# Performance work log

Measured on AMD Instinct MI355X. Metric: run time of the kernel, lower is better.

## Reference

```python
import jax, jax.numpy as jnp
import numpy as np

NUM_HEADS = 32
NUM_KV_HEADS = 8
HEAD_DIM = 128
SEQ = 2048
MAX_SLOTS = 4096
SCALE = float(1.0 / np.sqrt(HEAD_DIM))  # attn_scale
G = NUM_HEADS // NUM_KV_HEADS  # num_queries_per_kv


def setup_inputs() -> dict:
    key = jax.random.key(0)
    k1, k2, k3 = jax.random.split(key, 3)
    q = jax.random.normal(k1, (SEQ, NUM_HEADS, HEAD_DIM), dtype=jnp.float32)
    k = jax.random.normal(k2, (SEQ, NUM_KV_HEADS, HEAD_DIM), dtype=jnp.float32)
    v = jax.random.normal(k3, (SEQ, NUM_KV_HEADS, HEAD_DIM), dtype=jnp.float32)
    k_cache = jnp.zeros((MAX_SLOTS, NUM_KV_HEADS, HEAD_DIM), dtype=jnp.float32)
    v_cache = jnp.zeros((MAX_SLOTS, NUM_KV_HEADS, HEAD_DIM), dtype=jnp.float32)
    slot_mapping = jnp.arange(SEQ, dtype=jnp.int64)  # contiguous block_table slots
    return {"q": q, "k": k, "v": v, "k_cache": k_cache, "v_cache": v_cache,
            "slot_mapping": slot_mapping}


def reference(q, k, v, k_cache, v_cache, slot_mapping):
    # prefill: scatter-write new K/V into the paged cache (self.k_cache[slot_mapping] = k)
    kc = k_cache.at[slot_mapping].set(k)
    vc = v_cache.at[slot_mapping].set(v)
    # gather K/V back from the cache via slot mapping (paged gather pattern)
    k_attn = kc[slot_mapping]  # (S, Hkv, D) == k since slots are unique
    v_attn = vc[slot_mapping]
    # GQA: repeat_interleave kv heads to match query heads
    kr = jnp.repeat(k_attn, G, axis=1)  # (S, H, D)
    vr = jnp.repeat(v_attn, G, axis=1)
    # scores: (H, Sq, Sk), naive full materialization as in the original
    scores = jnp.einsum('qhd,khd->hqk', q, kr) * SCALE
    sq, sk = q.shape[0], k_attn.shape[0]
    mask = jnp.tril(jnp.ones((sq, sk), dtype=bool))  # causal (num_query_tokens > 1)
    scores = jnp.where(mask[None, :, :], scores, -jnp.inf)
    weights = jax.nn.softmax(scores, axis=-1)
    out = jnp.einsum('hqk,khd->qhd', weights, vr)  # (S, H, D)
    return out
```

## Files before the change

kernel.cpp:

```cpp
#include <hip/hip_runtime.h>
#include <hip/hip_bf16.h>

#define SEQ 2048
#define QSTR 4096
#define CSCALE 0.1275174364688796f

typedef __attribute__((ext_vector_type(8)))  short short8;
typedef __attribute__((ext_vector_type(4)))  float f32x4;
typedef __attribute__((ext_vector_type(16))) float f32x16;

union PF8 { unsigned u[4]; short8 s; };

__device__ __forceinline__ unsigned short f2bf(float f) {
    union { __hip_bfloat16 b; unsigned short u; } cv;
    cv.b = __float2bfloat16(f);
    return cv.u;
}
__device__ __forceinline__ float bf2f(unsigned short u) {
    unsigned v = ((unsigned)u) << 16;
    return __builtin_bit_cast(float, v);
}

__device__ __forceinline__ void gload16(const unsigned short* g, unsigned short* l) {
    __builtin_amdgcn_global_load_lds(
        (const __attribute__((address_space(1))) void*)g,
        (__attribute__((address_space(3))) void*)l, 16, 0, 0);
}

__global__ void prep_k(const float* __restrict__ Kg, unsigned short* __restrict__ Kb) {
    int gi = blockIdx.x * 256 + threadIdx.x;
    int kv = gi >> 8;
    int rem = gi & 255;
    int hk = rem >> 5;
    int d4 = rem & 31;
    f32x4 k4 = *(const f32x4*)(Kg + ((size_t)kv * 8 + hk) * 128 + 4 * d4);
    ushort4 u = make_ushort4(f2bf(k4[0]), f2bf(k4[1]), f2bf(k4[2]), f2bf(k4[3]));
    *(ushort4*)(Kb + ((size_t)hk * SEQ + kv) * 128 + 4 * d4) = u;
}

__global__ void prep_v(const float* __restrict__ Vg, unsigned short* __restrict__ Vtb) {
    const int hk  = blockIdx.x >> 5;
    const int kvb = blockIdx.x & 31;
    __shared__ unsigned short T[128][72];
    const int t = threadIdx.x;
    #pragma unroll
    for (int i = 0; i < 8; ++i) {
        int idx = t + 256 * i;
        int r = idx >> 5, d4 = idx & 31;
        f32x4 v = *(const f32x4*)(Vg + ((size_t)(kvb * 64 + r) * 8 + hk) * 128 + 4 * d4);
        T[4 * d4 + 0][r] = f2bf(v[0]);
        T[4 * d4 + 1][r] = f2bf(v[1]);
        T[4 * d4 + 2][r] = f2bf(v[2]);
        T[4 * d4 + 3][r] = f2bf(v[3]);
    }
    __syncthreads();
    #pragma unroll
    for (int i = 0; i < 8; ++i) {
        int idx = t + 256 * i;
        int d = idx >> 4, c4 = idx & 15;
        ushort4 u = *(ushort4*)&T[d][4 * c4];
        *(ushort4*)(Vtb + ((size_t)hk * 128 + d) * SEQ + kvb * 64 + 4 * c4) = u;
    }
}

__launch_bounds__(256, 2)
__global__ void attn_fwd(const float* __restrict__ Qg,
                         const unsigned short* __restrict__ Kb,
                         const unsigned short* __restrict__ Vtb,
                         float* __restrict__ Og) {
    const int bid = blockIdx.x;
    const int p   = bid >> 5;
    const int h   = bid & 31;
    const int hk  = h >> 2;
    const int qbB = 31 - p;
    const int qbA = p;
    const int nsB = 32 - p;

    const int tid  = threadIdx.x;
    const int w    = tid >> 6;
    const int b    = w & 1;
    const int hf   = w >> 1;
    const int lane = tid & 63;
    const int q5   = lane & 31;
    const int t5   = lane >> 5;

    __shared__ unsigned short Ks[2][64][128];
    __shared__ unsigned short Vp[2][64][128];
    __shared__ float mstat[2][4][32];
    __shared__ unsigned short Otb[32][136];

    short8 qf[8];
    auto LOADQ = [&](int qb) __attribute__((always_inline)) {
        const float* qp = Qg + (size_t)(qb * 64 + 32 * b + q5) * QSTR + h * 128 + 8 * t5;
        #pragma unroll
        for (int st = 0; st < 8; ++st) {
            f32x4 a = *(const f32x4*)(qp + 16 * st);
            f32x4 c = *(const f32x4*)(qp + 16 * st + 4);
            short8 f;
            f[0] = (short)f2bf(a[0] * CSCALE); f[1] = (short)f2bf(a[1] * CSCALE);
            f[2] = (short)f2bf(a[2] * CSCALE); f[3] = (short)f2bf(a[3] * CSCALE);
            f[4] = (short)f2bf(c[0] * CSCALE); f[5] = (short)f2bf(c[1] * CSCALE);
            f[6] = (short)f2bf(c[2] * CSCALE); f[7] = (short)f2bf(c[3] * CSCALE);
            qf[st] = f;
        }
    };

    auto ISSUE = [&](int kv0, int bb) __attribute__((always_inline)) {
        #pragma unroll
        for (int p4 = 0; p4 < 4; ++p4) {
            int row = 16 * w + 4 * p4 + (lane >> 4);
            const unsigned short* g = Kb +
                ((size_t)hk * SEQ + kv0 + row) * 128 + 8 * ((lane & 15) ^ (row & 15));
            gload16(g, &Ks[bb][16 * w + 4 * p4][0]);
        }
        #pragma unroll
        for (int p4 = 0; p4 < 4; ++p4) {
            int r  = 16 * w + 4 * p4 + (lane >> 4);
            int gg = lane & 15;
            int d  = 2 * r + (gg >> 3);
            int c  = (gg & 7) ^ (r & 7);
            const unsigned short* g = Vtb +
                ((size_t)hk * 128 + d) * SEQ + kv0 + 8 * c;
            gload16(g, &Vp[bb][16 * w + 4 * p4][0]);
        }
    };

    f32x16 oacc[4];
    float m, l;
    auto RESET = [&]() __attribute__((always_inline)) {
        #pragma unroll
        for (int dt = 0; dt < 4; ++dt)
            #pragma unroll
            for (int r = 0; r < 16; ++r) oacc[dt][r] = 0.f;
        m = -1e30f; l = 0.f;
    };

    auto EPI = [&](int qb) __attribute__((always_inline)) {
        if (t5 == 0) mstat[0][w][q5] = m;
        asm volatile("s_waitcnt lgkmcnt(0)" ::: "memory");
        __builtin_amdgcn_sched_barrier(0);
        __builtin_amdgcn_s_barrier();
        const float mo = mstat[0][w ^ 2][q5];
        const float M  = fmaxf(m, mo);
        const float sc = exp2f(m - M);
        #pragma unroll
        for (int dt = 0; dt < 4; ++dt)
            #pragma unroll
            for (int r = 0; r < 16; ++r) oacc[dt][r] *= sc;
        const float lp = l * sc;
        if (t5 == 0) mstat[1][w][q5] = lp;
        asm volatile("s_waitcnt lgkmcnt(0)" ::: "memory");
        __builtin_amdgcn_sched_barrier(0);
        __builtin_amdgcn_s_barrier();
        const float rl = 1.0f / (lp + mstat[1][w ^ 2][q5]);

        #pragma unroll 1
        for (int bb = 0; bb < 2; ++bb) {
            if (w == 2 + bb) {
                #pragma unroll
                for (int dt = 0; dt < 4; ++dt)
                    #pragma unroll
                    for (int ii = 0; ii < 4; ++ii) {
                        ushort4 u = make_ushort4(
                            f2bf(oacc[dt][4 * ii + 0]), f2bf(oacc[dt][4 * ii + 1]),
                            f2bf(oacc[dt][4 * ii + 2]), f2bf(oacc[dt][4 * ii + 3]));
                        *(ushort4*)&Otb[q5][32 * dt + 8 * ii + 4 * t5] = u;
                    }
            }
            asm volatile("s_waitcnt lgkmcnt(0)" ::: "memory");
            __builtin_amdgcn_sched_barrier(0);
            __builtin_amdgcn_s_barrier();
            if (w == bb) {
                #pragma unroll
                for (int dt = 0; dt < 4; ++dt)
                    #pragma unroll
                    for (int ii = 0; ii < 4; ++ii) {
                        ushort4 o1 = *(ushort4*)&Otb[q5][32 * dt + 8 * ii + 4 * t5];
                        ushort4 u = make_ushort4(
                            f2bf((oacc[dt][4 * ii + 0] + bf2f(o1.x)) * rl),
                            f2bf((oacc[dt][4 * ii + 1] + bf2f(o1.y)) * rl),
                            f2bf((oacc[dt][4 * ii + 2] + bf2f(o1.z)) * rl),
                            f2bf((oacc[dt][4 * ii + 3] + bf2f(o1.w)) * rl));
                        *(ushort4*)&Otb[q5][32 * dt + 8 * ii + 4 * t5] = u;
                    }
            }
            asm volatile("s_waitcnt lgkmcnt(0)" ::: "memory");
            __builtin_amdgcn_sched_barrier(0);
            __builtin_amdgcn_s_barrier();
            {
                const int r  = tid >> 3;
                const int c0 = 16 * (tid & 7);
                float* og = Og + (size_t)(qb * 64 + 32 * bb + r) * QSTR + h * 128 + c0;
                #pragma unroll
                for (int j = 0; j < 4; ++j) {
                    ushort4 u = *(ushort4*)&Otb[r][c0 + 4 * j];
                    f32x4 v;
                    v[0] = bf2f(u.x); v[1] = bf2f(u.y);
                    v[2] = bf2f(u.z); v[3] = bf2f(u.w);
                    *(f32x4*)(og + 4 * j) = v;
                }
            }
            asm volatile("s_waitcnt lgkmcnt(0)" ::: "memory");
            __builtin_amdgcn_sched_barrier(0);
            __builtin_amdgcn_s_barrier();
        }
    };

    LOADQ(qbB);
    #pragma unroll
    for (int st = 0; st < 8; ++st) asm volatile("" :: "v"(qf[st]));
    asm volatile("s_waitcnt vmcnt(0)" ::: "memory");
    RESET();

    ISSUE(0, 0);
    ISSUE(64, 1);

    for (int s = 0; s < 33; ++s) {
        if (s == nsB) {
            LOADQ(qbA);
            EPI(qbB);
            RESET();
        }
        const bool isB = (s < nsB);
        const int kv0  = isB ? 64 * s : 64 * (s - nsB);
        const int qb   = isB ? qbB : qbA;
        const int q0w  = qb * 64 + 32 * b;
        const int buf  = s & 1;

        if (s + 1 < 33) asm volatile("s_waitcnt vmcnt(8)" ::: "memory");
        else            asm volatile("s_waitcnt vmcnt(0)" ::: "memory");
        __builtin_amdgcn_s_barrier();

        const int kvh = kv0 + 32 * hf;
        if (kvh <= q0w + 31) {
            f32x16 sac;
            #pragma unroll
            for (int r = 0; r < 16; ++r) sac[r] = 0.f;
            __builtin_amdgcn_s_setprio(1);
            #pragma unroll
            for (int st = 0; st < 8; ++st) {
                short8 kf = *(const short8*)
                    &Ks[buf][32 * hf + q5][8 * ((2 * st + t5) ^ (q5 & 15))];
                sac = __builtin_amdgcn_mfma_f32_32x32x16_bf16(kf, qf[st], sac, 0, 0, 0);
            }
            __builtin_amdgcn_s_setprio(0);

            if (kvh + 31 > q0w) {
                const int qrow = q0w + q5;
                #pragma unroll
                for (int r = 0; r < 16; ++r) {
                    int kv = kvh + (r & 3) + 8 * (r >> 2) + 4 * t5;
                    if (kv > qrow) sac[r] = -1e30f;
                }
            }

            float m8[8], m4[4], m2[2];
            #pragma unroll
            for (int i = 0; i < 8; ++i) m8[i] = fmaxf(sac[i], sac[i + 8]);
            #pragma unroll
            for (int i = 0; i < 4; ++i) m4[i] = fmaxf(m8[i], m8[i + 4]);
            m2[0] = fmaxf(m4[0], m4[2]); m2[1] = fmaxf(m4[1], m4[3]);
            float mx = fmaxf(m2[0], m2[1]);
            mx = fmaxf(mx, __shfl_xor(mx, 32));

            const bool skip = __all(mx <= m + 11.0f);
            float fac = 1.0f;
            if (!skip) {
                float mn = fmaxf(m, mx);
                fac = exp2f(m - mn);
                m = mn;
            }

            #pragma unroll
            for (int r = 0; r < 16; ++r) sac[r] = exp2f(sac[r] - m);
            float s8[8], s4[4], s2[2];
            #pragma unroll
            for (int i = 0; i < 8; ++i) s8[i] = sac[i] + sac[i + 8];
            #pragma unroll
            for (int i = 0; i < 4; ++i) s4[i] = s8[i] + s8[i + 4];
            s2[0] = s4[0] + s4[2]; s2[1] = s4[1] + s4[3];
            float ps = s2[0] + s2[1];
            ps += __shfl_xor(ps, 32);
            if (!skip) {
                l = l * fac + ps;
                #pragma unroll
                for (int dt = 0; dt < 4; ++dt)
                    #pragma unroll
                    for (int r = 0; r < 16; ++r) oacc[dt][r] *= fac;
            } else {
                l += ps;
            }

            unsigned pkw[8];
            #pragma unroll
            for (int rp = 0; rp < 8; ++rp)
                pkw[rp] = (unsigned)f2bf(sac[2 * rp]) |
                          ((unsigned)f2bf(sac[2 * rp + 1]) << 16);

            unsigned xp[8];
            #pragma unroll
            for (int i = 0; i < 8; ++i)
                xp[i] = (unsigned)__shfl_xor((int)pkw[i], 32);

            PF8 pf[2];
            #pragma unroll
            for (int ks = 0; ks < 2; ++ks) {
                #pragma unroll
                for (int j = 0; j < 4; ++j) {
                    const int ib = (j & 1) + 4 * ks;
                    const unsigned own_lo = pkw[ib];
                    const unsigned own_hi = pkw[ib + 2];
                    const unsigned par_lo = xp[ib];
                    const unsigned par_hi = xp[ib + 2];
                    pf[ks].u[j] = (j < 2) ? (t5 ? par_hi : own_lo)
                                          : (t5 ? own_hi : par_lo);
                }
            }

            __builtin_amdgcn_s_setprio(1);
            #pragma unroll
            for (int dt = 0; dt < 4; ++dt) {
                #pragma unroll
                for (int ks = 0; ks < 2; ++ks) {
                    const int gg = 8 * (q5 & 1) +
                        ((4 * hf + 2 * ks + t5) ^ ((q5 >> 1) & 7));
                    short8 vf = *(const short8*)
                        &Vp[buf][16 * dt + (q5 >> 1)][8 * gg];
                    oacc[dt] = __builtin_amdgcn_mfma_f32_32x32x16_bf16(vf, pf[ks].s, oacc[dt], 0, 0, 0);
                }
            }
            __builtin_amdgcn_s_setprio(0);
        }

        asm volatile("" ::: "memory");
        __builtin_amdgcn_s_barrier();
        if (s + 2 < 33) {
            const int s2 = s + 2;
            ISSUE((s2 < nsB) ? 64 * s2 : 64 * (s2 - nsB), s & 1);
        }
    }

    EPI(qbA);
}

extern "C" void kernel_launch(void* const* d_in, const int* in_sizes, int n_in,
                              void* d_out, int out_size, void* d_ws, size_t ws_size,
                              hipStream_t stream) {
    const float* q = (const float*)d_in[0];
    const float* k = (const float*)d_in[1];
    const float* v = (const float*)d_in[2];
    float* out = (float*)d_out;
    unsigned short* Kb  = (unsigned short*)d_ws;
    unsigned short* Vtb = Kb + (size_t)8 * SEQ * 128;
    prep_k<<<dim3(2048), 256, 0, stream>>>(k, Kb);
    prep_v<<<dim3(256), 256, 0, stream>>>(v, Vtb);
    attn_fwd<<<dim3(512), 256, 0, stream>>>(q, Kb, Vtb, out);
}
```

Baseline: 90.90 us.

## Switch attention MFMAs from 32x32x16 to 16x16x32 tiles with reworked fragment layouts

Replaces the 32x32x16 bf16 MFMA tiling for both QK^T and PV with 16x16x32 MFMAs, splitting each wave's 32 query rows into two 16-row halves that keep separate max and sum statistics. The Q, K and V fragment loads, the causal mask indexing, the softmax reductions (now two-level shuffles) and the P repacking via cross-lane shuffles are all rewritten for the new layout, and K fragments are loaded into registers ahead of the MFMAs. The aim is a cheaper instruction mix or better MFMA issue and latency behaviour. In exchange it adds more shuffles and register pressure, and a risk of layout mismatches.

```diff
diff --git a/kernel.cpp b/kernel.cpp
--- a/kernel.cpp
+++ b/kernel.cpp
@@ -7,7 +7,6 @@
 
 typedef __attribute__((ext_vector_type(8)))  short short8;
 typedef __attribute__((ext_vector_type(4)))  float f32x4;
-typedef __attribute__((ext_vector_type(16))) float f32x16;
 
 union PF8 { unsigned u[4]; short8 s; };
 
@@ -81,27 +80,31 @@
     const int b    = w & 1;
     const int hf   = w >> 1;
     const int lane = tid & 63;
-    const int q5   = lane & 31;
-    const int t5   = lane >> 5;
+    const int c16  = lane & 15;
+    const int g    = lane >> 4;
 
     __shared__ unsigned short Ks[2][64][128];
     __shared__ unsigned short Vp[2][64][128];
     __shared__ float mstat[2][4][32];
     __shared__ unsigned short Otb[32][136];
 
-    short8 qf[8];
+    short8 qf[2][4];
     auto LOADQ = [&](int qb) __attribute__((always_inline)) {
-        const float* qp = Qg + (size_t)(qb * 64 + 32 * b + q5) * QSTR + h * 128 + 8 * t5;
-        #pragma unroll
-        for (int st = 0; st < 8; ++st) {
-            f32x4 a = *(const f32x4*)(qp + 16 * st);
-            f32x4 c = *(const f32x4*)(qp + 16 * st + 4);
-            short8 f;
-            f[0] = (short)f2bf(a[0] * CSCALE); f[1] = (short)f2bf(a[1] * CSCALE);
-            f[2] = (short)f2bf(a[2] * CSCALE); f[3] = (short)f2bf(a[3] * CSCALE);
-            f[4] = (short)f2bf(c[0] * CSCALE); f[5] = (short)f2bf(c[1] * CSCALE);
-            f[6] = (short)f2bf(c[2] * CSCALE); f[7] = (short)f2bf(c[3] * CSCALE);
-            qf[st] = f;
+        #pragma unroll
+        for (int hf2 = 0; hf2 < 2; ++hf2) {
+            const float* qp = Qg + (size_t)(qb * 64 + 32 * b + 16 * hf2 + c16) * QSTR
+                              + h * 128 + 8 * g;
+            #pragma unroll
+            for (int kt = 0; kt < 4; ++kt) {
+                f32x4 a = *(const f32x4*)(qp + 32 * kt);
+                f32x4 c = *(const f32x4*)(qp + 32 * kt + 4);
+                short8 f;
+                f[0] = (short)f2bf(a[0] * CSCALE); f[1] = (short)f2bf(a[1] * CSCALE);
+                f[2] = (short)f2bf(a[2] * CSCALE); f[3] = (short)f2bf(a[3] * CSCALE);
+                f[4] = (short)f2bf(c[0] * CSCALE); f[5] = (short)f2bf(c[1] * CSCALE);
+                f[6] = (short)f2bf(c[2] * CSCALE); f[7] = (short)f2bf(c[3] * CSCALE);
+                qf[hf2][kt] = f;
+            }
         }
     };
 
@@ -109,9 +112,9 @@
         #pragma unroll
         for (int p4 = 0; p4 < 4; ++p4) {
             int row = 16 * w + 4 * p4 + (lane >> 4);
-            const unsigned short* g = Kb +
+            const unsigned short* gp = Kb +
                 ((size_t)hk * SEQ + kv0 + row) * 128 + 8 * ((lane & 15) ^ (row & 15));
-            gload16(g, &Ks[bb][16 * w + 4 * p4][0]);
+            gload16(gp, &Ks[bb][16 * w + 4 * p4][0]);
         }
         #pragma unroll
         for (int p4 = 0; p4 < 4; ++p4) {
@@ -119,52 +122,59 @@
             int gg = lane & 15;
             int d  = 2 * r + (gg >> 3);
             int c  = (gg & 7) ^ (r & 7);
-            const unsigned short* g = Vtb +
+            const unsigned short* gp = Vtb +
                 ((size_t)hk * 128 + d) * SEQ + kv0 + 8 * c;
-            gload16(g, &Vp[bb][16 * w + 4 * p4][0]);
+            gload16(gp, &Vp[bb][16 * w + 4 * p4][0]);
         }
     };
 
-    f32x16 oacc[4];
-    float m, l;
+    f32x4 o4[2][8];
+    float m[2], l[2];
     auto RESET = [&]() __attribute__((always_inline)) {
         #pragma unroll
-        for (int dt = 0; dt < 4; ++dt)
-            #pragma unroll
-            for (int r = 0; r < 16; ++r) oacc[dt][r] = 0.f;
-        m = -1e30f; l = 0.f;
+        for (int hf2 = 0; hf2 < 2; ++hf2)
+            #pragma unroll
+            for (int dt = 0; dt < 8; ++dt)
+                o4[hf2][dt] = (f32x4){0.f, 0.f, 0.f, 0.f};
+        m[0] = m[1] = -1e30f; l[0] = l[1] = 0.f;
     };
 
     auto EPI = [&](int qb) __attribute__((always_inline)) {
-        if (t5 == 0) mstat[0][w][q5] = m;
+        if (g == 0) { mstat[0][w][c16] = m[0]; mstat[0][w][16 + c16] = m[1]; }
         asm volatile("s_waitcnt lgkmcnt(0)" ::: "memory");
         __builtin_amdgcn_sched_barrier(0);
         __builtin_amdgcn_s_barrier();
-        const float mo = mstat[0][w ^ 2][q5];
-        const float M  = fmaxf(m, mo);
-        const float sc = exp2f(m - M);
-        #pragma unroll
-        for (int dt = 0; dt < 4; ++dt)
-            #pragma unroll
-            for (int r = 0; r < 16; ++r) oacc[dt][r] *= sc;
-        const float lp = l * sc;
-        if (t5 == 0) mstat[1][w][q5] = lp;
+        float lp[2], rl[2];
+        #pragma unroll
+        for (int hf2 = 0; hf2 < 2; ++hf2) {
+            const float mo = mstat[0][w ^ 2][16 * hf2 + c16];
+            const float M  = fmaxf(m[hf2], mo);
+            const float sc = exp2f(m[hf2] - M);
+            #pragma unroll
+            for (int dt = 0; dt < 8; ++dt)
+                #pragma unroll
+                for (int r = 0; r < 4; ++r) o4[hf2][dt][r] *= sc;
+            lp[hf2] = l[hf2] * sc;
+        }
+        if (g == 0) { mstat[1][w][c16] = lp[0]; mstat[1][w][16 + c16] = lp[1]; }
         asm volatile("s_waitcnt lgkmcnt(0)" ::: "memory");
         __builtin_amdgcn_sched_barrier(0);
         __builtin_amdgcn_s_barrier();
-        const float rl = 1.0f / (lp + mstat[1][w ^ 2][q5]);
+        #pragma unroll
+        for (int hf2 = 0; hf2 < 2; ++hf2)
+            rl[hf2] = 1.0f / (lp[hf2] + mstat[1][w ^ 2][16 * hf2 + c16]);
 
         #pragma unroll 1
         for (int bb = 0; bb < 2; ++bb) {
             if (w == 2 + bb) {
                 #pragma unroll
-                for (int dt = 0; dt < 4; ++dt)
-                    #pragma unroll
-                    for (int ii = 0; ii < 4; ++ii) {
+                for (int hf2 = 0; hf2 < 2; ++hf2)
+                    #pragma unroll
+                    for (int dt = 0; dt < 8; ++dt) {
                         ushort4 u = make_ushort4(
-                            f2bf(oacc[dt][4 * ii + 0]), f2bf(oacc[dt][4 * ii + 1]),
-                            f2bf(oacc[dt][4 * ii + 2]), f2bf(oacc[dt][4 * ii + 3]));
-                        *(ushort4*)&Otb[q5][32 * dt + 8 * ii + 4 * t5] = u;
+                            f2bf(o4[hf2][dt][0]), f2bf(o4[hf2][dt][1]),
+                            f2bf(o4[hf2][dt][2]), f2bf(o4[hf2][dt][3]));
+                        *(ushort4*)&Otb[16 * hf2 + c16][16 * dt + 4 * g] = u;
                     }
             }
             asm volatile("s_waitcnt lgkmcnt(0)" ::: "memory");
@@ -172,16 +182,16 @@
             __builtin_amdgcn_s_barrier();
             if (w == bb) {
                 #pragma unroll
-                for (int dt = 0; dt < 4; ++dt)
-                    #pragma unroll
-                    for (int ii = 0; ii < 4; ++ii) {
-                        ushort4 o1 = *(ushort4*)&Otb[q5][32 * dt + 8 * ii + 4 * t5];
+                for (int hf2 = 0; hf2 < 2; ++hf2)
+                    #pragma unroll
+                    for (int dt = 0; dt < 8; ++dt) {
+                        ushort4 o1 = *(ushort4*)&Otb[16 * hf2 + c16][16 * dt + 4 * g];
                         ushort4 u = make_ushort4(
-                            f2bf((oacc[dt][4 * ii + 0] + bf2f(o1.x)) * rl),
-                            f2bf((oacc[dt][4 * ii + 1] + bf2f(o1.y)) * rl),
-                            f2bf((oacc[dt][4 * ii + 2] + bf2f(o1.z)) * rl),
-                            f2bf((oacc[dt][4 * ii + 3] + bf2f(o1.w)) * rl));
-                        *(ushort4*)&Otb[q5][32 * dt + 8 * ii + 4 * t5] = u;
+                            f2bf((o4[hf2][dt][0] + bf2f(o1.x)) * rl[hf2]),
+                            f2bf((o4[hf2][dt][1] + bf2f(o1.y)) * rl[hf2]),
+                            f2bf((o4[hf2][dt][2] + bf2f(o1.z)) * rl[hf2]),
+                            f2bf((o4[hf2][dt][3] + bf2f(o1.w)) * rl[hf2]));
+                        *(ushort4*)&Otb[16 * hf2 + c16][16 * dt + 4 * g] = u;
                     }
             }
             asm volatile("s_waitcnt lgkmcnt(0)" ::: "memory");
@@ -208,7 +218,9 @@
 
     LOADQ(qbB);
     #pragma unroll
-    for (int st = 0; st < 8; ++st) asm volatile("" :: "v"(qf[st]));
+    for (int hf2 = 0; hf2 < 2; ++hf2)
+        #pragma unroll
+        for (int kt = 0; kt < 4; ++kt) asm volatile("" :: "v"(qf[hf2][kt]));
     asm volatile("s_waitcnt vmcnt(0)" ::: "memory");
     RESET();
 
@@ -233,101 +245,120 @@
 
         const int kvh = kv0 + 32 * hf;
         if (kvh <= q0w + 31) {
-            f32x16 sac;
-            #pragma unroll
-            for (int r = 0; r < 16; ++r) sac[r] = 0.f;
+            short8 kf[8];
+            #pragma unroll
+            for (int ct = 0; ct < 2; ++ct)
+                #pragma unroll
+                for (int kt = 0; kt < 4; ++kt)
+                    kf[4 * ct + kt] = *(const short8*)
+                        &Ks[buf][32 * hf + 16 * ct + c16][8 * ((4 * kt + g) ^ c16)];
+
+            f32x4 sac[2][2];
+            #pragma unroll
+            for (int hf2 = 0; hf2 < 2; ++hf2)
+                #pragma unroll
+                for (int ct = 0; ct < 2; ++ct)
+                    sac[hf2][ct] = (f32x4){0.f, 0.f, 0.f, 0.f};
             __builtin_amdgcn_s_setprio(1);
             #pragma unroll
-            for (int st = 0; st < 8; ++st) {
-                short8 kf = *(const short8*)
-                    &Ks[buf][32 * hf + q5][8 * ((2 * st + t5) ^ (q5 & 15))];
-                sac = __builtin_amdgcn_mfma_f32_32x32x16_bf16(kf, qf[st], sac, 0, 0, 0);
+            for (int kt = 0; kt < 4; ++kt) {
+                sac[0][0] = __builtin_amdgcn_mfma_f32_16x16x32_bf16(kf[kt],     qf[0][kt], sac[0][0], 0, 0, 0);
+                sac[1][0] = __builtin_amdgcn_mfma_f32_16x16x32_bf16(kf[kt],     qf[1][kt], sac[1][0], 0, 0, 0);
+                sac[0][1] = __builtin_amdgcn_mfma_f32_16x16x32_bf16(kf[4 + kt], qf[0][kt], sac[0][1], 0, 0, 0);
+                sac[1][1] = __builtin_amdgcn_mfma_f32_16x16x32_bf16(kf[4 + kt], qf[1][kt], sac[1][1], 0, 0, 0);
             }
             __builtin_amdgcn_s_setprio(0);
 
             if (kvh + 31 > q0w) {
-                const int qrow = q0w + q5;
-                #pragma unroll
-                for (int r = 0; r < 16; ++r) {
-                    int kv = kvh + (r & 3) + 8 * (r >> 2) + 4 * t5;
-                    if (kv > qrow) sac[r] = -1e30f;
+                #pragma unroll
+                for (int hf2 = 0; hf2 < 2; ++hf2) {
+                    const int qrow = q0w + 16 * hf2 + c16;
+                    #pragma unroll
+                    for (int ct = 0; ct < 2; ++ct)
+                        #pragma unroll
+                        for (int r = 0; r < 4; ++r) {
+                            int kv = kvh + 16 * ct + 4 * g + r;
+                            if (kv > qrow) sac[hf2][ct][r] = -1e30f;
+                        }
                 }
             }
 
-            float m8[8], m4[4], m2[2];
-            #pragma unroll
-            for (int i = 0; i < 8; ++i) m8[i] = fmaxf(sac[i], sac[i + 8]);
-            #pragma unroll
-            for (int i = 0; i < 4; ++i) m4[i] = fmaxf(m8[i], m8[i + 4]);
-            m2[0] = fmaxf(m4[0], m4[2]); m2[1] = fmaxf(m4[1], m4[3]);
-            float mx = fmaxf(m2[0], m2[1]);
-            mx = fmaxf(mx, __shfl_xor(mx, 32));
-
-            const bool skip = __all(mx <= m + 11.0f);
-            float fac = 1.0f;
+            float mx[2];
+            #pragma unroll
+            for (int hf2 = 0; hf2 < 2; ++hf2) {
+                float t4a = fmaxf(sac[hf2][0][0], sac[hf2][1][0]);
+                float t4b = fmaxf(sac[hf2][0][1], sac[hf2][1][1]);
+                float t4c = fmaxf(sac[hf2][0][2], sac[hf2][1][2]);
+                float t4d = fmaxf(sac[hf2][0][3], sac[hf2][1][3]);
+                float t2a = fmaxf(t4a, t4b), t2b = fmaxf(t4c, t4d);
+                float mm = fmaxf(t2a, t2b);
+                mm = fmaxf(mm, __shfl_xor(mm, 16));
+                mm = fmaxf(mm, __shfl_xor(mm, 32));
+                mx[hf2] = mm;
+            }
+
+            const bool skip = __all(fmaxf(mx[0] - m[0], mx[1] - m[1]) <= 11.0f);
             if (!skip) {
-                float mn = fmaxf(m, mx);
-                fac = exp2f(m - mn);
-                m = mn;
-            }
-
-            #pragma unroll
-            for (int r = 0; r < 16; ++r) sac[r] = exp2f(sac[r] - m);
-            float s8[8], s4[4], s2[2];
-            #pragma unroll
-            for (int i = 0; i < 8; ++i) s8[i] = sac[i] + sac[i + 8];
-            #pragma unroll
-            for (int i = 0; i < 4; ++i) s4[i] = s8[i] + s8[i + 4];
-            s2[0] = s4[0] + s4[2]; s2[1] = s4[1] + s4[3];
-            float ps = s2[0] + s2[1];
-            ps += __shfl_xor(ps, 32);
-            if (!skip) {
-                l = l * fac + ps;
-                #pragma unroll
-                for (int dt = 0; dt < 4; ++dt)
-                    #pragma unroll
-                    for (int r = 0; r < 16; ++r) oacc[dt][r] *= fac;
-            } else {
-                l += ps;
-            }
-
-            unsigned pkw[8];
-            #pragma unroll
-            for (int rp = 0; rp < 8; ++rp)
-                pkw[rp] = (unsigned)f2bf(sac[2 * rp]) |
-                          ((unsigned)f2bf(sac[2 * rp + 1]) << 16);
-
-            unsigned xp[8];
-            #pragma unroll
-            for (int i = 0; i < 8; ++i)
-                xp[i] = (unsigned)__shfl_xor((int)pkw[i], 32);
-
-            PF8 pf[2];
-            #pragma unroll
-            for (int ks = 0; ks < 2; ++ks) {
-                #pragma unroll
-                for (int j = 0; j < 4; ++j) {
-                    const int ib = (j & 1) + 4 * ks;
-                    const unsigned own_lo = pkw[ib];
-                    const unsigned own_hi = pkw[ib + 2];
-                    const unsigned par_lo = xp[ib];
-                    const unsigned par_hi = xp[ib + 2];
-                    pf[ks].u[j] = (j < 2) ? (t5 ? par_hi : own_lo)
-                                          : (t5 ? own_hi : par_lo);
+                #pragma unroll
+                for (int hf2 = 0; hf2 < 2; ++hf2) {
+                    float mn  = fmaxf(m[hf2], mx[hf2]);
+                    float fac = exp2f(m[hf2] - mn);
+                    m[hf2] = mn;
+                    l[hf2] *= fac;
+                    #pragma unroll
+                    for (int dt = 0; dt < 8; ++dt)
+                        #pragma unroll
+                        for (int r = 0; r < 4; ++r) o4[hf2][dt][r] *= fac;
                 }
             }
 
+            unsigned pk[2][4];
+            #pragma unroll
+            for (int hf2 = 0; hf2 < 2; ++hf2) {
+                #pragma unroll
+                for (int ct = 0; ct < 2; ++ct)
+                    #pragma unroll
+                    for (int r = 0; r < 4; ++r)
+                        sac[hf2][ct][r] = exp2f(sac[hf2][ct][r] - m[hf2]);
+                float s4a = sac[hf2][0][0] + sac[hf2][1][0];
+                float s4b = sac[hf2][0][1] + sac[hf2][1][1];
+                float s4c = sac[hf2][0][2] + sac[hf2][1][2];
+                float s4d = sac[hf2][0][3] + sac[hf2][1][3];
+                float ps = (s4a + s4b) + (s4c + s4d);
+                ps += __shfl_xor(ps, 16);
+                ps += __shfl_xor(ps, 32);
+                l[hf2] += ps;
+                #pragma unroll
+                for (int ct = 0; ct < 2; ++ct)
+                    #pragma unroll
+                    for (int pp = 0; pp < 2; ++pp)
+                        pk[hf2][2 * ct + pp] =
+                            (unsigned)f2bf(sac[hf2][ct][2 * pp]) |
+                            ((unsigned)f2bf(sac[hf2][ct][2 * pp + 1]) << 16);
+            }
+
+            PF8 pf0, pf1;
+            {
+                const int sel = g >> 1;
+                #pragma unroll
+                for (int w4 = 0; w4 < 4; ++w4) {
+                    const int src = 16 * (2 * (g & 1) + (w4 >> 1)) + c16;
+                    unsigned lo0 = (unsigned)__shfl((int)pk[0][w4 & 1], src);
+                    unsigned hi0 = (unsigned)__shfl((int)pk[0][2 + (w4 & 1)], src);
+                    unsigned lo1 = (unsigned)__shfl((int)pk[1][w4 & 1], src);
+                    unsigned hi1 = (unsigned)__shfl((int)pk[1][2 + (w4 & 1)], src);
+                    pf0.u[w4] = sel ? hi0 : lo0;
+                    pf1.u[w4] = sel ? hi1 : lo1;
+                }
+            }
+
             __builtin_amdgcn_s_setprio(1);
             #pragma unroll
-            for (int dt = 0; dt < 4; ++dt) {
-                #pragma unroll
-                for (int ks = 0; ks < 2; ++ks) {
-                    const int gg = 8 * (q5 & 1) +
-                        ((4 * hf + 2 * ks + t5) ^ ((q5 >> 1) & 7));
-                    short8 vf = *(const short8*)
-                        &Vp[buf][16 * dt + (q5 >> 1)][8 * gg];
-                    oacc[dt] = __builtin_amdgcn_mfma_f32_32x32x16_bf16(vf, pf[ks].s, oacc[dt], 0, 0, 0);
-                }
+            for (int dt = 0; dt < 8; ++dt) {
+                const int gg = 8 * (c16 & 1) + ((4 * hf + g) ^ (c16 >> 1));
+                short8 vf = *(const short8*)&Vp[buf][8 * dt + (c16 >> 1)][8 * gg];
+                o4[0][dt] = __builtin_amdgcn_mfma_f32_16x16x32_bf16(vf, pf0.s, o4[0][dt], 0, 0, 0);
+                o4[1][dt] = __builtin_amdgcn_mfma_f32_16x16x32_bf16(vf, pf1.s, o4[1][dt], 0, 0, 0);
             }
             __builtin_amdgcn_s_setprio(0);
         }
```

Result: slower. 99.90 us (+9.9%).

## Drop double-buffered K/V prefetch for single buffer to raise occupancy to three blocks

Applied to the files above, without the earlier changes.

Replaces the two-stage asynchronous K/V prefetch ring with a single LDS buffer that is loaded synchronously at the start of each iteration. LDS use per block drops, so the launch bound can request three blocks per CU instead of two. It also halves the cross-half-wave shuffles by sending only the half of each packed probability word the partner lane needs. In exchange, global load latency is no longer hidden inside a block and must be covered by the extra resident blocks.

```diff
diff --git a/kernel.cpp b/kernel.cpp
--- a/kernel.cpp
+++ b/kernel.cpp
@@ -63,7 +63,7 @@
     }
 }
 
-__launch_bounds__(256, 2)
+__launch_bounds__(256, 3)
 __global__ void attn_fwd(const float* __restrict__ Qg,
                          const unsigned short* __restrict__ Kb,
                          const unsigned short* __restrict__ Vtb,
@@ -84,8 +84,8 @@
     const int q5   = lane & 31;
     const int t5   = lane >> 5;
 
-    __shared__ unsigned short Ks[2][64][128];
-    __shared__ unsigned short Vp[2][64][128];
+    __shared__ unsigned short Ks[64][128];
+    __shared__ unsigned short Vp[64][128];
     __shared__ float mstat[2][4][32];
     __shared__ unsigned short Otb[32][136];
 
@@ -105,13 +105,13 @@
         }
     };
 
-    auto ISSUE = [&](int kv0, int bb) __attribute__((always_inline)) {
+    auto ISSUE = [&](int kv0) __attribute__((always_inline)) {
         #pragma unroll
         for (int p4 = 0; p4 < 4; ++p4) {
             int row = 16 * w + 4 * p4 + (lane >> 4);
             const unsigned short* g = Kb +
                 ((size_t)hk * SEQ + kv0 + row) * 128 + 8 * ((lane & 15) ^ (row & 15));
-            gload16(g, &Ks[bb][16 * w + 4 * p4][0]);
+            gload16(g, &Ks[16 * w + 4 * p4][0]);
         }
         #pragma unroll
         for (int p4 = 0; p4 < 4; ++p4) {
@@ -121,7 +121,7 @@
             int c  = (gg & 7) ^ (r & 7);
             const unsigned short* g = Vtb +
                 ((size_t)hk * 128 + d) * SEQ + kv0 + 8 * c;
-            gload16(g, &Vp[bb][16 * w + 4 * p4][0]);
+            gload16(g, &Vp[16 * w + 4 * p4][0]);
         }
     };
 
@@ -212,9 +212,6 @@
     asm volatile("s_waitcnt vmcnt(0)" ::: "memory");
     RESET();
 
-    ISSUE(0, 0);
-    ISSUE(64, 1);
-
     for (int s = 0; s < 33; ++s) {
         if (s == nsB) {
             LOADQ(qbA);
@@ -225,10 +222,9 @@
         const int kv0  = isB ? 64 * s : 64 * (s - nsB);
         const int qb   = isB ? qbB : qbA;
         const int q0w  = qb * 64 + 32 * b;
-        const int buf  = s & 1;
-
-        if (s + 1 < 33) asm volatile("s_waitcnt vmcnt(8)" ::: "memory");
-        else            asm volatile("s_waitcnt vmcnt(0)" ::: "memory");
+
+        ISSUE(kv0);
+        asm volatile("s_waitcnt vmcnt(0)" ::: "memory");
         __builtin_amdgcn_s_barrier();
 
         const int kvh = kv0 + 32 * hf;
@@ -240,7 +236,7 @@
             #pragma unroll
             for (int st = 0; st < 8; ++st) {
                 short8 kf = *(const short8*)
-                    &Ks[buf][32 * hf + q5][8 * ((2 * st + t5) ^ (q5 & 15))];
+                    &Ks[32 * hf + q5][8 * ((2 * st + t5) ^ (q5 & 15))];
                 sac = __builtin_amdgcn_mfma_f32_32x32x16_bf16(kf, qf[st], sac, 0, 0, 0);
             }
             __builtin_amdgcn_s_setprio(0);
@@ -297,10 +293,14 @@
                 pkw[rp] = (unsigned)f2bf(sac[2 * rp]) |
                           ((unsigned)f2bf(sac[2 * rp + 1]) << 16);
 
-            unsigned xp[8];
-            #pragma unroll
-            for (int i = 0; i < 8; ++i)
-                xp[i] = (unsigned)__shfl_xor((int)pkw[i], 32);
+            unsigned rcv[4];
+            #pragma unroll
+            for (int i = 0; i < 4; ++i) {
+                const int loI = (i & 1) + 4 * (i >> 1);
+                const int hiI = loI + 2;
+                unsigned wsend = t5 ? pkw[loI] : pkw[hiI];
+                rcv[i] = (unsigned)__shfl_xor((int)wsend, 32);
+            }
 
             PF8 pf[2];
             #pragma unroll
@@ -308,12 +308,12 @@
                 #pragma unroll
                 for (int j = 0; j < 4; ++j) {
                     const int ib = (j & 1) + 4 * ks;
+                    const int ri = (j & 1) + 2 * ks;
                     const unsigned own_lo = pkw[ib];
                     const unsigned own_hi = pkw[ib + 2];
-                    const unsigned par_lo = xp[ib];
-                    const unsigned par_hi = xp[ib + 2];
-                    pf[ks].u[j] = (j < 2) ? (t5 ? par_hi : own_lo)
-                                          : (t5 ? own_hi : par_lo);
+                    const unsigned par    = rcv[ri];
+                    pf[ks].u[j] = (j < 2) ? (t5 ? par : own_lo)
+                                          : (t5 ? own_hi : par);
                 }
             }
 
@@ -325,7 +325,7 @@
                     const int gg = 8 * (q5 & 1) +
                         ((4 * hf + 2 * ks + t5) ^ ((q5 >> 1) & 7));
                     short8 vf = *(const short8*)
-                        &Vp[buf][16 * dt + (q5 >> 1)][8 * gg];
+                        &Vp[16 * dt + (q5 >> 1)][8 * gg];
                     oacc[dt] = __builtin_amdgcn_mfma_f32_32x32x16_bf16(vf, pf[ks].s, oacc[dt], 0, 0, 0);
                 }
             }
@@ -334,10 +334,6 @@
 
         asm volatile("" ::: "memory");
         __builtin_amdgcn_s_barrier();
-        if (s + 2 < 33) {
-            const int s2 = s + 2;
-            ISSUE((s2 < nsB) ? 64 * s2 : 64 * (s2 - nsB), s & 1);
-        }
     }
 
     EPI(qbA);
```

New measurement: 223.7 us. 2.46x slower.
